# Kernel tuning notes

Hardware: AMD Instinct MI355X
Metric: run time of the kernel (lower is better)

The kernel has to match this reference:

```python
import jax, jax.numpy as jnp
import numpy as np

EPS = 1e-5
P = 8  # patch size


def ln_chan(x, w, b):
    # LayerNorm over channel dim C of (B,C,H,W): per-pixel mean/var across channels
    mu = x.mean(axis=1, keepdims=True)
    var = x.var(axis=1, keepdims=True)
    return (x - mu) / jnp.sqrt(var + EPS) * w[None, :, None, None] + b[None, :, None, None]


def conv1x1(x, w):
    # w: (O, C) -> pointwise conv
    return jnp.einsum('bchw,oc->bohw', x, w)


def dwconv3(x, w):
    # depthwise 3x3, SAME padding; w: (C,1,3,3)
    return jax.lax.conv_general_dilated(
        x, w, window_strides=(1, 1), padding='SAME',
        dimension_numbers=('NCHW', 'OIHW', 'NCHW'),
        feature_group_count=x.shape[1])


def to_patches(t):
    b, c, h, w = t.shape
    return t.reshape(b, c, h // P, P, w // P, P).transpose(0, 1, 2, 4, 3, 5)


def from_patches(t, h, w):
    b, c = t.shape[:2]
    return t.transpose(0, 1, 2, 4, 3, 5).reshape(b, c, h, w)


def setup_inputs() -> dict:
    key = jax.random.key(0)
    ks = jax.random.split(key, 8)
    B, C, H, W = 4, 64, 256, 256
    s = 0.1  # weight scale to keep activations sane
    inp = {
        'x': jax.random.normal(ks[0], (B, C, H, W), jnp.float32),
        'evt': jax.random.normal(ks[1], (B, C, H, W), jnp.float32),
        'w_q': jax.random.normal(ks[2], (2 * C, C), jnp.float32) * s,
        'w_kv': jax.random.normal(ks[3], (4 * C, C), jnp.float32) * s,
        'w_qdw': jax.random.normal(ks[4], (2 * C, 1, 3, 3), jnp.float32) * s,
        'w_kvdw': jax.random.normal(ks[5], (4 * C, 1, 3, 3), jnp.float32) * s,
        'w_proj': jax.random.normal(ks[6], (C, 2 * C), jnp.float32) * s,
        'ln_img_w': jnp.ones((C,), jnp.float32),
        'ln_img_b': jnp.zeros((C,), jnp.float32),
        'ln_evt_w': jnp.ones((C,), jnp.float32),
        'ln_evt_b': jnp.zeros((C,), jnp.float32),
        'ln_out_w': jnp.ones((2 * C,), jnp.float32),
        'ln_out_b': jnp.zeros((2 * C,), jnp.float32),
    }
    return inp


def reference(x, evt, w_q, w_kv, w_qdw, w_kvdw, w_proj,
              ln_img_w, ln_img_b, ln_evt_w, ln_evt_b, ln_out_w, ln_out_b):
    x = ln_chan(x, ln_img_w, ln_img_b)
    evt = ln_chan(evt, ln_evt_w, ln_evt_b)
    q = dwconv3(conv1x1(x, w_q), w_qdw)          # (B, 2C, H, W)
    kv = dwconv3(conv1x1(evt, w_kv), w_kvdw)     # (B, 4C, H, W)
    k, v = jnp.split(kv, 2, axis=1)
    h, w = q.shape[-2:]
    q_fft = jnp.fft.rfft2(to_patches(q))         # (B,2C,h/8,w/8,8,5) complex
    k_fft = jnp.fft.rfft2(to_patches(k))
    out = jnp.fft.irfft2(q_fft * k_fft, s=(P, P))
    out = from_patches(out, h, w)                # (B, 2C, H, W)
    out = ln_chan(out, ln_out_w, ln_out_b)
    out = v * out
    return conv1x1(out, w_proj)                  # (B, C, H, W)
```

## Files before the change

kernel.cpp:

```cpp
#include <hip/hip_runtime.h>

typedef __attribute__((ext_vector_type(8))) short bf16x8;
typedef __attribute__((ext_vector_type(4))) float f32x4;
typedef __attribute__((ext_vector_type(2))) float f32x2;
typedef __attribute__((ext_vector_type(4))) unsigned int u32x4;
typedef __attribute__((ext_vector_type(2))) unsigned int u32x2;

__device__ __forceinline__ unsigned short f2bf(float f) {
    union { float f; unsigned int u; } v; v.f = f;
    return (unsigned short)((v.u + 0x7fffu + ((v.u >> 16) & 1u)) >> 16);
}
__device__ __forceinline__ float bflo(unsigned int u) {
    union { unsigned int u; float f; } v; v.u = u << 16; return v.f;
}
__device__ __forceinline__ float bfhi(unsigned int u) {
    union { unsigned int u; float f; } v; v.u = u & 0xffff0000u; return v.f;
}
__device__ __forceinline__ f32x2 bfpair(unsigned int u) {
    union { unsigned int u; float f; } lo, hi;
    lo.u = u << 16; hi.u = u & 0xffff0000u;
    return (f32x2){lo.f, hi.f};
}

__device__ __forceinline__ float wred_allsum(float x) {
    asm volatile(
        "s_nop 1\n\t"
        "v_add_f32_dpp %0, %0, %0 row_shr:1 bound_ctrl:0\n\t"
        "s_nop 1\n\t"
        "v_add_f32_dpp %0, %0, %0 row_shr:2 bound_ctrl:0\n\t"
        "s_nop 1\n\t"
        "v_add_f32_dpp %0, %0, %0 row_shr:4 bound_ctrl:0\n\t"
        "s_nop 1\n\t"
        "v_add_f32_dpp %0, %0, %0 row_shr:8 bound_ctrl:0\n\t"
        "s_nop 1\n\t"
        "v_add_f32_dpp %0, %0, %0 row_bcast:15 row_mask:0xa bound_ctrl:0\n\t"
        "s_nop 1\n\t"
        "v_add_f32_dpp %0, %0, %0 row_bcast:31 row_mask:0xc bound_ctrl:0\n\t"
        "s_nop 1"
        : "+v"(x));
    return __builtin_bit_cast(float, __builtin_amdgcn_readlane(__builtin_bit_cast(int, x), 63));
}

__global__ __launch_bounds__(256, 8)
void ln_kernel(const float* __restrict__ x, const float* __restrict__ evt,
               const float* __restrict__ lwx, const float* __restrict__ lbx,
               const float* __restrict__ lwe, const float* __restrict__ lbe,
               unsigned short* __restrict__ xo, unsigned short* __restrict__ eo)
{
    __shared__ float xt[64][68];
    __shared__ float ps[4][64], ps2[4][64];
    __shared__ float smu[64], sinv[64], slw[64], slb[64];

    const int tid = threadIdx.x;
    const int z = blockIdx.z, b = blockIdx.y;
    const int hw0 = blockIdx.x * 64;
    const float* src = z ? evt : x;
    const float* lw  = z ? lwe : lwx;
    const float* lb  = z ? lbe : lbx;
    unsigned short* dst = z ? eo : xo;

    if (tid < 64) { slw[tid] = lw[tid]; slb[tid] = lb[tid]; }

    const float* sp = src + (size_t)b * 64 * 65536 + hw0;
    #pragma unroll
    for (int it = 0; it < 4; ++it) {
        int i = tid + it * 256;
        int c = i >> 4, p4 = i & 15;
        f32x4 v = *(const f32x4*)&sp[(size_t)c * 65536 + p4 * 4];
        xt[p4 * 4 + 0][c] = v.x;
        xt[p4 * 4 + 1][c] = v.y;
        xt[p4 * 4 + 2][c] = v.z;
        xt[p4 * 4 + 3][c] = v.w;
    }
    __syncthreads();

    {
        int px = tid & 63, part = tid >> 6;
        float s = 0.f, s2 = 0.f;
        #pragma unroll
        for (int j = 0; j < 4; ++j) {
            f32x4 v = *(const f32x4*)&xt[px][part * 16 + j * 4];
            s  += v.x + v.y + v.z + v.w;
            s2 += v.x * v.x + v.y * v.y + v.z * v.z + v.w * v.w;
        }
        ps[part][px] = s; ps2[part][px] = s2;
    }
    __syncthreads();
    if (tid < 64) {
        float s  = ps[0][tid] + ps[1][tid] + ps[2][tid] + ps[3][tid];
        float s2 = ps2[0][tid] + ps2[1][tid] + ps2[2][tid] + ps2[3][tid];
        float mu = s * (1.f / 64.f);
        smu[tid] = mu;
        sinv[tid] = rsqrtf(s2 * (1.f / 64.f) - mu * mu + 1e-5f);
    }
    __syncthreads();

    unsigned short* dp = dst + ((size_t)b * 65536 + hw0) * 64;
    #pragma unroll
    for (int it = 0; it < 2; ++it) {
        int i = tid + it * 256;
        int px = i >> 3, oct = i & 7;
        float mu = smu[px], inv = sinv[px];
        f32x4 v0 = *(const f32x4*)&xt[px][oct * 8];
        f32x4 v1 = *(const f32x4*)&xt[px][oct * 8 + 4];
        u32x4 w;
        int c = oct * 8;
        float a0 = (v0.x - mu) * inv * slw[c + 0] + slb[c + 0];
        float a1 = (v0.y - mu) * inv * slw[c + 1] + slb[c + 1];
        w[0] = (unsigned int)f2bf(a0) | ((unsigned int)f2bf(a1) << 16);
        a0 = (v0.z - mu) * inv * slw[c + 2] + slb[c + 2];
        a1 = (v0.w - mu) * inv * slw[c + 3] + slb[c + 3];
        w[1] = (unsigned int)f2bf(a0) | ((unsigned int)f2bf(a1) << 16);
        a0 = (v1.x - mu) * inv * slw[c + 4] + slb[c + 4];
        a1 = (v1.y - mu) * inv * slw[c + 5] + slb[c + 5];
        w[2] = (unsigned int)f2bf(a0) | ((unsigned int)f2bf(a1) << 16);
        a0 = (v1.z - mu) * inv * slw[c + 6] + slb[c + 6];
        a1 = (v1.w - mu) * inv * slw[c + 7] + slb[c + 7];
        w[3] = (unsigned int)f2bf(a0) | ((unsigned int)f2bf(a1) << 16);
        *(u32x4*)&dp[(size_t)px * 64 + oct * 8] = w;
    }
}

#define PR_WB    14336
#define PR_WDW   30720
#define PR_SMEM  35328

__global__ __launch_bounds__(512, 8)
void prod_kernel(const unsigned short* __restrict__ src,
                 const float* __restrict__ wmat, const float* __restrict__ wdw,
                 unsigned short* __restrict__ dst)
{
    __shared__ __align__(16) char smem[PR_SMEM];
    unsigned short* A   = (unsigned short*)(smem);
    unsigned short* Wb  = (unsigned short*)(smem + PR_WB);
    unsigned short* pre = (unsigned short*)(smem);
    float* swdw = (float*)(smem + PR_WDW);

    const int tid = threadIdx.x;
    const int pj = blockIdx.x, pi = blockIdx.y, b = blockIdx.z;
    const int h0 = pi * 8, w0 = pj * 8;

    #pragma unroll
    for (int it = 0; it < 4; ++it) {
        int i = tid + it * 512;
        int o = i >> 4, c4 = i & 15;
        f32x4 wv = *(const f32x4*)&wmat[o * 64 + c4 * 4];
        unsigned int lo = (unsigned int)f2bf(wv[0]) | ((unsigned int)f2bf(wv[1]) << 16);
        unsigned int hi = (unsigned int)f2bf(wv[2]) | ((unsigned int)f2bf(wv[3]) << 16);
        u32x2 pk = {lo, hi};
        *(u32x2*)&Wb[o * 64 + (((c4 >> 1) ^ (o & 7)) << 3) + (c4 & 1) * 4] = pk;
    }
    for (int i = tid; i < 1152; i += 512) swdw[i] = wdw[i];
    for (int i = tid; i < 768; i += 512) A[6400 + i] = 0;
    #pragma unroll
    for (int it = 0; it < 2; ++it) {
        int i = tid + it * 512;
        if (i < 800) {
            int px = i >> 3, oct = i & 7;
            int r = px / 10, cc = px - r * 10;
            int gh = h0 - 1 + r, gw = w0 - 1 + cc;
            u32x4 val = {0u, 0u, 0u, 0u};
            if (gh >= 0 && gh < 256 && gw >= 0 && gw < 256)
                val = *(const u32x4*)&src[((size_t)(b * 65536 + gh * 256 + gw)) * 64 + oct * 8];
            *(u32x4*)&A[px * 64 + ((oct ^ (px & 7)) << 3)] = val;
        }
    }
    __syncthreads();

    const int lane = tid & 63;
    const int l15 = lane & 15, l4 = lane >> 4;
    const int o_n = (tid >> 6) * 16 + l15;
    f32x4 acc[7];
    #pragma unroll
    for (int mt = 0; mt < 7; ++mt) acc[mt] = (f32x4){0.f, 0.f, 0.f, 0.f};
    #pragma unroll
    for (int ks = 0; ks < 2; ++ks) {
        int cch = ks * 4 + l4;
        bf16x8 bfrag = *(const bf16x8*)&Wb[o_n * 64 + ((cch ^ (o_n & 7)) << 3)];
        #pragma unroll
        for (int mt = 0; mt < 7; ++mt) {
            int px = mt * 16 + l15;
            bf16x8 afrag = *(const bf16x8*)&A[px * 64 + ((cch ^ (px & 7)) << 3)];
            acc[mt] = __builtin_amdgcn_mfma_f32_16x16x32_bf16(afrag, bfrag, acc[mt], 0, 0, 0);
        }
    }
    __syncthreads();

    #pragma unroll
    for (int mt = 0; mt < 7; ++mt)
        #pragma unroll
        for (int r = 0; r < 4; ++r) {
            int px = mt * 16 + l4 * 4 + r;
            if (px < 100)
                pre[px * 128 + (((o_n >> 3) ^ (px & 7)) << 3) + (o_n & 7)] = f2bf(acc[mt][r]);
        }
    __syncthreads();

    {
        const int o = (tid & 63) * 2;
        const int och = o >> 3, osub = o & 7;
        const int pc = tid >> 6;
        f32x2 wdp[9];
        #pragma unroll
        for (int t = 0; t < 9; ++t)
            wdp[t] = (f32x2){swdw[o * 9 + t], swdw[o * 9 + 9 + t]};
        const size_t patchbase = ((size_t)(b * 32 + pi) * 32 + pj) * 8192;

        f32x2 ra[3], rb[3], rc[3];
        #define LOADROW(dstv, rr)                                                        \
            {                                                                            \
                _Pragma("unroll")                                                        \
                for (int d = 0; d < 3; ++d) {                                            \
                    int hp = (rr) * 10 + pc + d;                                         \
                    unsigned int u = *(const unsigned int*)                              \
                        &pre[hp * 128 + ((och ^ (hp & 7)) << 3) + osub];                 \
                    dstv[d] = bfpair(u);                                                 \
                }                                                                        \
            }
        LOADROW(ra, 0)
        LOADROW(rb, 1)
        #pragma unroll
        for (int r = 2; r < 10; ++r) {
            LOADROW(rc, r)
            f32x2 s = ra[0] * wdp[0];
            s += ra[1] * wdp[1]; s += ra[2] * wdp[2];
            s += rb[0] * wdp[3]; s += rb[1] * wdp[4]; s += rb[2] * wdp[5];
            s += rc[0] * wdp[6]; s += rc[1] * wdp[7]; s += rc[2] * wdp[8];
            int px = (r - 2) * 8 + pc;
            unsigned int outw = (unsigned int)f2bf(s.x) | ((unsigned int)f2bf(s.y) << 16);
            *(unsigned int*)&dst[patchbase + px * 128 + o] = outw;
            #pragma unroll
            for (int d = 0; d < 3; ++d) { ra[d] = rb[d]; rb[d] = rc[d]; }
        }
        #undef LOADROW
    }
}

#define PK_Q    0
#define PK_K    16384
#define PK_WP   32768
#define PK_LW   49152
#define PK_LB   49664
#define PK_SMEM 50176

__global__ __launch_bounds__(512, 6)
void patch_kernel(const unsigned short* __restrict__ qb,
                  const unsigned short* __restrict__ kb,
                  const unsigned short* __restrict__ vb,
                  const float* __restrict__ w_proj,
                  const float* __restrict__ lnw, const float* __restrict__ lnb,
                  float* __restrict__ out)
{
    __shared__ __align__(16) char smem[PK_SMEM];
    unsigned short* sq  = (unsigned short*)(smem + PK_Q);
    unsigned short* sk  = (unsigned short*)(smem + PK_K);
    unsigned short* sy  = sq;
    unsigned short* sv  = sk;
    float*          sc  = (float*)(smem + PK_K);
    unsigned short* swp = (unsigned short*)(smem + PK_WP);
    float* slw = (float*)(smem + PK_LW);
    float* slb = (float*)(smem + PK_LB);

    const int tid = threadIdx.x;
    const int tj = blockIdx.x, ti = blockIdx.y, b = blockIdx.z;
    const int h0 = ti * 8, w0 = tj * 8;
    const size_t pbase = ((size_t)(b * 32 + ti) * 32 + tj) * 8192;

    u32x4 vreg0 = *(const u32x4*)&vb[pbase + tid * 16];
    u32x4 vreg1 = *(const u32x4*)&vb[pbase + tid * 16 + 8];

    if (tid < 128) { slw[tid] = lnw[tid]; slb[tid] = lnb[tid]; }
    #pragma unroll
    for (int it = 0; it < 2; ++it) {
        int i = tid + it * 512;
        *(u32x4*)&sq[i * 8] = *(const u32x4*)&qb[pbase + i * 8];
        *(u32x4*)&sk[i * 8] = *(const u32x4*)&kb[pbase + i * 8];
    }
    #pragma unroll
    for (int it = 0; it < 4; ++it) {
        int i = tid + it * 512;
        int o = i >> 5, c4 = i & 31;
        f32x4 wv = *(const f32x4*)&w_proj[o * 128 + c4 * 4];
        unsigned int lo = (unsigned int)f2bf(wv[0]) | ((unsigned int)f2bf(wv[1]) << 16);
        unsigned int hi = (unsigned int)f2bf(wv[2]) | ((unsigned int)f2bf(wv[3]) << 16);
        u32x2 pk = {lo, hi};
        *(u32x2*)&swp[o * 128 + (((c4 >> 1) ^ (o & 7)) << 3) + (c4 & 1) * 4] = pk;
    }
    __syncthreads();

    const int pr = tid >> 6;
    const int cq = tid & 63;
    const float lw0 = slw[2 * cq], lw1 = slw[2 * cq + 1];
    const float lb0 = slb[2 * cq], lb1 = slb[2 * cq + 1];

    f32x2 acc[8];
    #pragma unroll
    for (int pc = 0; pc < 8; ++pc) acc[pc] = (f32x2){0.f, 0.f};
    #pragma unroll
    for (int tr = 0; tr < 8; ++tr) {
        int rrow = (pr - tr) & 7;
        f32x2 kv[8];
        #pragma unroll
        for (int j = 0; j < 8; ++j)
            kv[j] = bfpair(*(const unsigned int*)&sk[(rrow * 8 + j) * 128 + cq * 2]);
        #pragma unroll
        for (int tc = 0; tc < 8; ++tc) {
            f32x2 qv = bfpair(*(const unsigned int*)&sq[(tr * 8 + tc) * 128 + cq * 2]);
            #pragma unroll
            for (int pc = 0; pc < 8; ++pc)
                acc[pc] += qv * kv[(pc - tc) & 7];
        }
    }
    __syncthreads();

    *(u32x4*)&sv[tid * 16]     = vreg0;
    *(u32x4*)&sv[tid * 16 + 8] = vreg1;

    float mu[8], inv[8];
    #pragma unroll
    for (int pc = 0; pc < 8; ++pc) {
        float s  = wred_allsum(acc[pc].x + acc[pc].y);
        float s2 = wred_allsum(acc[pc].x * acc[pc].x + acc[pc].y * acc[pc].y);
        float m_ = s * (1.f / 128.f);
        mu[pc]  = m_;
        inv[pc] = rsqrtf(s2 * (1.f / 128.f) - m_ * m_ + 1e-5f);
    }
    __syncthreads();

    #pragma unroll
    for (int pc = 0; pc < 8; ++pc) {
        int px = pr * 8 + pc;
        unsigned int uv = *(const unsigned int*)&sv[px * 128 + cq * 2];
        float y0 = ((acc[pc].x - mu[pc]) * inv[pc] * lw0 + lb0) * bflo(uv);
        float y1 = ((acc[pc].y - mu[pc]) * inv[pc] * lw1 + lb1) * bfhi(uv);
        unsigned int pk = (unsigned int)f2bf(y0) | ((unsigned int)f2bf(y1) << 16);
        *(unsigned int*)&sy[px * 128 + (((cq >> 2) ^ (px & 7)) << 3) + 2 * (cq & 3)] = pk;
    }
    __syncthreads();

    {
        const int lane = tid & 63;
        const int l15 = lane & 15, l4 = lane >> 4;
        const int wave = tid >> 6;
        const int mt = wave >> 1;
        const int nt0 = 2 * (wave & 1);
        f32x4 pacc[2];
        pacc[0] = (f32x4){0.f, 0.f, 0.f, 0.f};
        pacc[1] = (f32x4){0.f, 0.f, 0.f, 0.f};
        const int px_a = mt * 16 + l15;
        #pragma unroll
        for (int ks = 0; ks < 4; ++ks) {
            int cch = ks * 4 + l4;
            bf16x8 af = *(const bf16x8*)&sy[px_a * 128 + ((cch ^ (px_a & 7)) << 3)];
            #pragma unroll
            for (int p2 = 0; p2 < 2; ++p2) {
                int o_n = (nt0 + p2) * 16 + l15;
                bf16x8 bfr = *(const bf16x8*)&swp[o_n * 128 + ((cch ^ (o_n & 7)) << 3)];
                pacc[p2] = __builtin_amdgcn_mfma_f32_16x16x32_bf16(af, bfr, pacc[p2], 0, 0, 0);
            }
        }
        #pragma unroll
        for (int p2 = 0; p2 < 2; ++p2)
            #pragma unroll
            for (int r = 0; r < 4; ++r) {
                int px = mt * 16 + l4 * 4 + r;
                int o = (nt0 + p2) * 16 + l15;
                sc[px * 64 + o] = pacc[p2][r];
            }
    }
    __syncthreads();

    {
        const int o = tid & 63, r = tid >> 6;
        float v0[4], v1[4];
        #pragma unroll
        for (int j = 0; j < 4; ++j) {
            v0[j] = sc[(r * 8 + j) * 64 + o];
            v1[j] = sc[(r * 8 + 4 + j) * 64 + o];
        }
        int obase = ((b * 64 + o) * 256 + h0 + r) * 256 + w0;
        *(f32x4*)&out[obase]     = (f32x4){v0[0], v0[1], v0[2], v0[3]};
        *(f32x4*)&out[obase + 4] = (f32x4){v1[0], v1[1], v1[2], v1[3]};
    }
}

extern "C" void kernel_launch(void* const* d_in, const int* in_sizes, int n_in,
                              void* d_out, int out_size, void* d_ws, size_t ws_size,
                              hipStream_t stream) {
    (void)in_sizes; (void)n_in; (void)out_size; (void)ws_size;
    const float* x        = (const float*)d_in[0];
    const float* evt      = (const float*)d_in[1];
    const float* w_q      = (const float*)d_in[2];
    const float* w_kv     = (const float*)d_in[3];
    const float* w_qdw    = (const float*)d_in[4];
    const float* w_kvdw   = (const float*)d_in[5];
    const float* w_proj   = (const float*)d_in[6];
    const float* ln_img_w = (const float*)d_in[7];
    const float* ln_img_b = (const float*)d_in[8];
    const float* ln_evt_w = (const float*)d_in[9];
    const float* ln_evt_b = (const float*)d_in[10];
    const float* ln_out_w = (const float*)d_in[11];
    const float* ln_out_b = (const float*)d_in[12];
    float* out = (float*)d_out;

    const size_t NPATCH = (size_t)4 * 32 * 32 * 8192;
    const size_t NLN    = (size_t)4 * 65536 * 64;
    unsigned short* qd  = (unsigned short*)d_ws;
    unsigned short* kd  = qd + NPATCH;
    unsigned short* eln = kd + NPATCH;
    unsigned short* xln = eln + NLN;
    unsigned short* vd  = xln;

    dim3 lgrid(1024, 4, 2), lblk(256);
    ln_kernel<<<lgrid, lblk, 0, stream>>>(x, evt, ln_img_w, ln_img_b,
                                          ln_evt_w, ln_evt_b, xln, eln);
    dim3 grid(32, 32, 4), blk(512);
    prod_kernel<<<grid, blk, 0, stream>>>(xln, w_q,            w_qdw,           qd);
    prod_kernel<<<grid, blk, 0, stream>>>(eln, w_kv,           w_kvdw,          kd);
    prod_kernel<<<grid, blk, 0, stream>>>(eln, w_kv + 128*64,  w_kvdw + 128*9,  vd);
    patch_kernel<<<grid, blk, 0, stream>>>(qd, kd, vd, w_proj, ln_out_w, ln_out_b, out);
}
```

Measured before the change: 264.7 us.

## Store patch intermediates channel-major with XOR swizzle and use packed FMA

The producer kernel now stages its depthwise-conv outputs in LDS and transposes them, so each thread writes two 16-byte channel-major rows with a swizzled pixel slot instead of scattered 4-byte stores. The patch kernel reads q, k and v in that channel-major layout using 16-byte vector loads. This removes the v staging through LDS and one barrier, and does the circular convolution with explicit v_pk_fma_f32. It adds an extra LDS round-trip and barrier in the producer, and producer and consumer must agree on the new swizzled layout.

```diff
diff --git a/kernel.cpp b/kernel.cpp
--- a/kernel.cpp
+++ b/kernel.cpp
@@ -20,6 +20,9 @@
     union { unsigned int u; float f; } lo, hi;
     lo.u = u << 16; hi.u = u & 0xffff0000u;
     return (f32x2){lo.f, hi.f};
+}
+__device__ __forceinline__ void pkfma(f32x2& d, f32x2 a, f32x2 b) {
+    asm("v_pk_fma_f32 %0, %1, %2, %0" : "+v"(d) : "v"(a), "v"(b));
 }
 
 __device__ __forceinline__ float wred_allsum(float x) {
@@ -196,6 +199,7 @@
         }
     __syncthreads();
 
+    f32x2 res[8];
     {
         const int o = (tid & 63) * 2;
         const int och = o >> 3, osub = o & 7;
@@ -204,7 +208,6 @@
         #pragma unroll
         for (int t = 0; t < 9; ++t)
             wdp[t] = (f32x2){swdw[o * 9 + t], swdw[o * 9 + 9 + t]};
-        const size_t patchbase = ((size_t)(b * 32 + pi) * 32 + pj) * 8192;
 
         f32x2 ra[3], rb[3], rc[3];
         #define LOADROW(dstv, rr)                                                        \
@@ -226,13 +229,46 @@
             s += ra[1] * wdp[1]; s += ra[2] * wdp[2];
             s += rb[0] * wdp[3]; s += rb[1] * wdp[4]; s += rb[2] * wdp[5];
             s += rc[0] * wdp[6]; s += rc[1] * wdp[7]; s += rc[2] * wdp[8];
-            int px = (r - 2) * 8 + pc;
-            unsigned int outw = (unsigned int)f2bf(s.x) | ((unsigned int)f2bf(s.y) << 16);
-            *(unsigned int*)&dst[patchbase + px * 128 + o] = outw;
+            res[r - 2] = s;
             #pragma unroll
             for (int d = 0; d < 3; ++d) { ra[d] = rb[d]; rb[d] = rc[d]; }
         }
         #undef LOADROW
+    }
+    __syncthreads();
+
+    {
+        unsigned short* ldout = (unsigned short*)smem;
+        const int o = (tid & 63) * 2;
+        const int pc = tid >> 6;
+        const int key = pc << 4;
+        #pragma unroll
+        for (int r = 0; r < 8; ++r) {
+            int px = r * 8 + pc;
+            unsigned int pk = (unsigned int)f2bf(res[r].x) | ((unsigned int)f2bf(res[r].y) << 16);
+            *(unsigned int*)&ldout[px * 128 + (o ^ key)] = pk;
+        }
+    }
+    __syncthreads();
+
+    {
+        unsigned short* ldout = (unsigned short*)smem;
+        const int c0 = (tid & 63) * 2;
+        const int s = tid >> 6;
+        const int sl = s ^ (tid & 7);
+        const size_t patchbase = ((size_t)(b * 32 + pi) * 32 + pj) * 8192;
+        unsigned int rv[8];
+        #pragma unroll
+        for (int j = 0; j < 8; ++j)
+            rv[j] = *(const unsigned int*)&ldout[(8 * s + j) * 128 + (c0 ^ (j << 4))];
+        u32x4 lo, hi;
+        #pragma unroll
+        for (int d = 0; d < 4; ++d) {
+            lo[d] = (rv[2 * d] & 0xffffu) | (rv[2 * d + 1] << 16);
+            hi[d] = (rv[2 * d] >> 16) | (rv[2 * d + 1] & 0xffff0000u);
+        }
+        *(u32x4*)&dst[patchbase + (size_t)c0 * 64 + sl * 8]       = lo;
+        *(u32x4*)&dst[patchbase + (size_t)(c0 + 1) * 64 + sl * 8] = hi;
     }
 }
 
@@ -255,7 +291,6 @@
     unsigned short* sq  = (unsigned short*)(smem + PK_Q);
     unsigned short* sk  = (unsigned short*)(smem + PK_K);
     unsigned short* sy  = sq;
-    unsigned short* sv  = sk;
     float*          sc  = (float*)(smem + PK_K);
     unsigned short* swp = (unsigned short*)(smem + PK_WP);
     float* slw = (float*)(smem + PK_LW);
@@ -266,8 +301,12 @@
     const int h0 = ti * 8, w0 = tj * 8;
     const size_t pbase = ((size_t)(b * 32 + ti) * 32 + tj) * 8192;
 
-    u32x4 vreg0 = *(const u32x4*)&vb[pbase + tid * 16];
-    u32x4 vreg1 = *(const u32x4*)&vb[pbase + tid * 16 + 8];
+    const int pr = tid >> 6;
+    const int cq = tid & 63;
+    const int key = cq & 7;
+
+    u32x4 vreg0 = *(const u32x4*)&vb[pbase + (2 * cq) * 64 + ((pr ^ key) << 3)];
+    u32x4 vreg1 = *(const u32x4*)&vb[pbase + (2 * cq + 1) * 64 + ((pr ^ key) << 3)];
 
     if (tid < 128) { slw[tid] = lnw[tid]; slb[tid] = lnb[tid]; }
     #pragma unroll
@@ -288,8 +327,6 @@
     }
     __syncthreads();
 
-    const int pr = tid >> 6;
-    const int cq = tid & 63;
     const float lw0 = slw[2 * cq], lw1 = slw[2 * cq + 1];
     const float lb0 = slb[2 * cq], lb1 = slb[2 * cq + 1];
 
@@ -298,23 +335,30 @@
     for (int pc = 0; pc < 8; ++pc) acc[pc] = (f32x2){0.f, 0.f};
     #pragma unroll
     for (int tr = 0; tr < 8; ++tr) {
-        int rrow = (pr - tr) & 7;
-        f32x2 kv[8];
-        #pragma unroll
-        for (int j = 0; j < 8; ++j)
-            kv[j] = bfpair(*(const unsigned int*)&sk[(rrow * 8 + j) * 128 + cq * 2]);
+        const int qs = (tr ^ key) << 3;
+        u32x4 q0 = *(const u32x4*)&sq[(2 * cq) * 64 + qs];
+        u32x4 q1 = *(const u32x4*)&sq[(2 * cq + 1) * 64 + qs];
+        const int rrow = (pr - tr) & 7;
+        const int ksl = (rrow ^ key) << 3;
+        u32x4 k0 = *(const u32x4*)&sk[(2 * cq) * 64 + ksl];
+        u32x4 k1 = *(const u32x4*)&sk[(2 * cq + 1) * 64 + ksl];
+        f32x2 kp[8];
+        #pragma unroll
+        for (int d = 0; d < 4; ++d) {
+            kp[2 * d]     = (f32x2){bflo(k0[d]), bflo(k1[d])};
+            kp[2 * d + 1] = (f32x2){bfhi(k0[d]), bfhi(k1[d])};
+        }
         #pragma unroll
         for (int tc = 0; tc < 8; ++tc) {
-            f32x2 qv = bfpair(*(const unsigned int*)&sq[(tr * 8 + tc) * 128 + cq * 2]);
+            const int d = tc >> 1;
+            f32x2 qp = (tc & 1) ? (f32x2){bfhi(q0[d]), bfhi(q1[d])}
+                                : (f32x2){bflo(q0[d]), bflo(q1[d])};
             #pragma unroll
             for (int pc = 0; pc < 8; ++pc)
-                acc[pc] += qv * kv[(pc - tc) & 7];
-        }
-    }
-    __syncthreads();
-
-    *(u32x4*)&sv[tid * 16]     = vreg0;
-    *(u32x4*)&sv[tid * 16 + 8] = vreg1;
+                pkfma(acc[pc], qp, kp[(pc - tc) & 7]);
+        }
+    }
+    __syncthreads();
 
     float mu[8], inv[8];
     #pragma unroll
@@ -325,14 +369,15 @@
         mu[pc]  = m_;
         inv[pc] = rsqrtf(s2 * (1.f / 128.f) - m_ * m_ + 1e-5f);
     }
-    __syncthreads();
 
     #pragma unroll
     for (int pc = 0; pc < 8; ++pc) {
         int px = pr * 8 + pc;
-        unsigned int uv = *(const unsigned int*)&sv[px * 128 + cq * 2];
-        float y0 = ((acc[pc].x - mu[pc]) * inv[pc] * lw0 + lb0) * bflo(uv);
-        float y1 = ((acc[pc].y - mu[pc]) * inv[pc] * lw1 + lb1) * bfhi(uv);
+        const int d = pc >> 1;
+        f32x2 vp = (pc & 1) ? (f32x2){bfhi(vreg0[d]), bfhi(vreg1[d])}
+                            : (f32x2){bflo(vreg0[d]), bflo(vreg1[d])};
+        float y0 = ((acc[pc].x - mu[pc]) * inv[pc] * lw0 + lb0) * vp.x;
+        float y1 = ((acc[pc].y - mu[pc]) * inv[pc] * lw1 + lb1) * vp.y;
         unsigned int pk = (unsigned int)f2bf(y0) | ((unsigned int)f2bf(y1) << 16);
         *(unsigned int*)&sy[px * 128 + (((cq >> 2) ^ (px & 7)) << 3) + 2 * (cq & 3)] = pk;
     }
```

Measured after the change: 282.4 us. 6.7% more time.
